# Kernel tuning notes

Hardware: AMD Instinct MI355X
Metric: run time of the kernel (lower is better)

## Reference

```python
import jax, jax.numpy as jnp
import numpy as np

DEPTH = 17                 # levels of the complete binary tree
N = 2**DEPTH - 1           # 131071 nodes, BFS order: children of n are 2n+1, 2n+2
IN_DIM = 128
HID = 128
OUT = 128


def setup_inputs() -> dict:
    key = jax.random.key(0)
    ks = jax.random.split(key, 20)

    def lin_w(k, o, i):
        s = 1.0 / np.sqrt(i)
        return jax.random.uniform(k, (o, i), minval=-s, maxval=s, dtype=jnp.float32)

    def lin_b(k, o, i):
        s = 1.0 / np.sqrt(i)
        return jax.random.uniform(k, (o,), minval=-s, maxval=s, dtype=jnp.float32)

    inp = {"x": jax.random.normal(ks[0], (N, IN_DIM), dtype=jnp.float32)}
    # complete binary tree, parent -> child edges (row0=src/parent, row1=dst/child)
    child = np.arange(1, N)
    parent = (child - 1) // 2
    inp["edge_index"] = jnp.asarray(np.stack([parent, child]), dtype=jnp.int32)
    names = [("Wi", "bWi", IN_DIM), ("Ui", "bUi", HID),
             ("Wf", "bWf", IN_DIM), ("Uf", "bUf", HID),
             ("Wo", "bWo", IN_DIM), ("Uo", "bUo", HID),
             ("Wu", "bWu", IN_DIM), ("Uu", "bUu", HID)]
    ki = 1
    for wname, bname, idim in names:
        inp[wname] = lin_w(ks[ki], HID, idim)
        inp[bname] = lin_b(ks[ki + 1], HID, idim)
        ki += 2
    inp["Wp"] = lin_w(ks[17], OUT, HID)
    inp["bWp"] = lin_b(ks[18], OUT, HID)
    return inp


def reference(x, edge_index, Wi, bWi, Ui, bUi, Wf, bWf, Uf, bUf,
              Wo, bWo, Uo, bUo, Wu, bWu, Uu, bUu, Wp, bWp):
    # edge_index encodes the complete binary tree in BFS order (children of n
    # are 2n+1 and 2n+2), so the recursion batches exactly by tree level.
    # Precompute input-side gate projections for ALL nodes in 4 GEMMs
    # (equivalent to calling W_*(x[node]) per node in the torch recursion).
    xi = x @ Wi.T + bWi            # (N, H)
    xf = x @ Wf.T + bWf
    xo = x @ Wo.T + bWo
    xu = x @ Wu.T + bWu

    h_next = None  # hidden states of the level below (children)
    c_next = None
    for d in range(DEPTH - 1, -1, -1):   # bottom-up over tree levels
        s = 2**d - 1                     # first node index of level d
        cnt = 2**d                       # nodes at level d
        li, lf, lo, lu = xi[s:s + cnt], xf[s:s + cnt], xo[s:s + cnt], xu[s:s + cnt]
        if h_next is None:               # leaves: no children, h_sum = 0
            i = jax.nn.sigmoid(li)
            o = jax.nn.sigmoid(lo)
            u = jnp.tanh(lu)
            c = i * u
        else:
            # children of node s+k are at positions 2(s+k)+1, 2(s+k)+2: contiguous
            ch_h = h_next.reshape(cnt, 2, HID)
            ch_c = c_next.reshape(cnt, 2, HID)
            h_sum = ch_h.sum(axis=1)     # child-sum
            i = jax.nn.sigmoid(li + h_sum @ Ui.T + bUi)
            o = jax.nn.sigmoid(lo + h_sum @ Uo.T + bUo)
            u = jnp.tanh(lu + h_sum @ Uu.T + bUu)
            # per-child forget gates: sigmoid(W_f x + U_f h_k)
            f = jax.nn.sigmoid(lf[:, None, :] + jnp.einsum('nkh,gh->nkg', ch_h, Uf) + bUf)
            c = i * u + (f * ch_c).sum(axis=1)
        h = o * jnp.tanh(c)
        h_next, c_next = h, c

    h_root = h_next[0]                   # root node index 0
    # dropout is identity in eval mode
    return h_root @ Wp.T + bWp           # (OUT,)
```

## Files before the change

### kernel.cpp

```cpp
#include <hip/hip_runtime.h>
#include <hip/hip_bf16.h>


#define DEPTH 17
#define NTREE ((1 << DEPTH) - 1)
#define DIM 128
#define XSTR 136
#define HSTR 136
#define CSTR 132

typedef __attribute__((ext_vector_type(8))) short short8;
typedef __attribute__((ext_vector_type(4))) float float4v;

__device__ __forceinline__ float sigm(float v) {
    return __fdividef(1.0f, 1.0f + __expf(-v));
}
__device__ __forceinline__ float ftanh(float v) {
    float e = __expf(2.0f * v);
    return 1.0f - __fdividef(2.0f, e + 1.0f);
}

__device__ __forceinline__ unsigned short f2bf(float f) {
    __bf16 h = (__bf16)f;
    unsigned short r;
    __builtin_memcpy(&r, &h, 2);
    return r;
}
__device__ __forceinline__ float bf2f(unsigned short s) {
    union { unsigned u; float f; } a; a.u = ((unsigned)s) << 16;
    return a.f;
}

struct WPtrs {
    const float* W[4];  const float* U[4];
    const float* bW[4]; const float* bU[4];
};

__global__ __launch_bounds__(256) void prep_kernel(WPtrs p, unsigned short* __restrict__ Bsw,
                                                   float* __restrict__ biasWU, float* __restrict__ biasL) {
    int idx = blockIdx.x * 256 + threadIdx.x;
    int j = idx & 7;
    int lane = (idx >> 3) & 63;
    int g = (idx >> 9) & 3;
    int ks = (idx >> 11) & 7;
    int w = idx >> 14;
    int L = lane & 15, q = lane >> 4;
    int c = w * 16 + L;
    int k = ks * 32 + q * 8 + j;
    float v = (k < 128) ? p.W[g][c * 128 + k] * (g == 3 ? 1.0f : 0.5f)
                        : p.U[g][c * 128 + (k - 128)];
    Bsw[idx] = f2bf(v);
    if (idx < 512) {
        int gg = idx >> 7, cc = idx & 127;
        biasWU[idx] = p.bW[gg][cc] + p.bU[gg][cc];
        biasL[idx]  = p.bW[gg][cc];
    }
}

__global__ __launch_bounds__(512, 2) void kd3_kernel(
    const float* __restrict__ x, const unsigned short* __restrict__ Bsw,
    const float* __restrict__ biasL, const float* __restrict__ biasWU,
    unsigned short* __restrict__ hbf, float* __restrict__ cbuf, int ntiles) {
    __shared__ __align__(16) unsigned short xs[2][56 * XSTR];
    __shared__ __align__(16) unsigned short h0[32 * XSTR];
    __shared__ __align__(16) unsigned short c0[32 * XSTR];
    __shared__ __align__(16) unsigned short h1[16 * XSTR];
    __shared__ __align__(16) unsigned short c1[16 * XSTR];
    __shared__ __align__(16) unsigned short hA2[8 * XSTR];
    __shared__ __align__(16) float cA2[8 * CSTR];

    const int tid = threadIdx.x;
    const int w = tid >> 6, lane = tid & 63, L = lane & 15, q = lane >> 4;
    const int ch = w * 16 + L;

    short8 b[32];
#pragma unroll
    for (int t = 0; t < 32; ++t)
        b[t] = *(const short8*)(Bsw + ((size_t)w << 14) + (t << 9) + lane * 8);

    float4 pfx[4];
    {
        const long tt = blockIdx.x;
#pragma unroll
        for (int k = 0; k < 4; ++k) {
            const int i = tid + 512 * k;
            if (i < 1792) {
                const int row = i >> 5, j = i & 31;
                const long node = (row < 32) ? (65535l + tt * 32 + row)
                                 : (row < 48) ? (32767l + tt * 16 + (row - 32))
                                              : (16383l + tt * 8 + (row - 48));
                pfx[k] = *(const float4*)(x + (size_t)node * DIM + j * 4);
            }
        }
    }

    for (int it = 0; it < ntiles; ++it) {
        const long tt = (long)it * gridDim.x + blockIdx.x;
        const int pc = it & 1;
        unsigned short* xsp = xs[pc];

#pragma unroll
        for (int k = 0; k < 4; ++k) {
            const int i = tid + 512 * k;
            if (i < 1792) {
                const int row = i >> 5, j = i & 31;
                ushort4 o;
                o.x = f2bf(pfx[k].x); o.y = f2bf(pfx[k].y);
                o.z = f2bf(pfx[k].z); o.w = f2bf(pfx[k].w);
                *(ushort4*)(xsp + row * XSTR + j * 4) = o;
            }
        }
        __syncthreads();

        if (it + 1 < ntiles) {
            const long tn = tt + gridDim.x;
#pragma unroll
            for (int k = 0; k < 4; ++k) {
                const int i = tid + 512 * k;
                if (i < 1792) {
                    const int row = i >> 5, j = i & 31;
                    const long node = (row < 32) ? (65535l + tn * 32 + row)
                                     : (row < 48) ? (32767l + tn * 16 + (row - 32))
                                                  : (16383l + tn * 8 + (row - 48));
                    pfx[k] = *(const float4*)(x + (size_t)node * DIM + j * 4);
                }
            }
        }

        if (it > 0) {
            const long pn2 = 16383l + (tt - gridDim.x) * 8;
            for (int i = tid; i < 8 * 16; i += 512) {
                const int row = i >> 4, g = i & 15;
                *(uint4*)(hbf + (size_t)(pn2 + row) * DIM + g * 8) = *(const uint4*)(hA2 + row * XSTR + g * 8);
            }
            for (int i = tid; i < 8 * 32; i += 512) {
                const int row = i >> 5, j = i & 31;
                *(float4*)(cbuf + (size_t)(pn2 + row) * DIM + j * 4) = *(const float4*)(cA2 + row * CSTR + j * 4);
            }
        }

        {
            float4v acc[2][3];
#pragma unroll
            for (int mm = 0; mm < 2; ++mm)
#pragma unroll
                for (int g = 0; g < 3; ++g) acc[mm][g] = (float4v){0.f, 0.f, 0.f, 0.f};
#pragma unroll
            for (int ks = 0; ks < 4; ++ks) {
                short8 a[2];
                a[0] = *(const short8*)(xsp + L * XSTR + ks * 32 + q * 8);
                a[1] = *(const short8*)(xsp + (16 + L) * XSTR + ks * 32 + q * 8);
#pragma unroll
                for (int g = 0; g < 3; ++g)
#pragma unroll
                    for (int mm = 0; mm < 2; ++mm)
                        acc[mm][g] = __builtin_amdgcn_mfma_f32_16x16x32_bf16(a[mm], b[ks * 4 + g], acc[mm][g], 0, 0, 0);
            }
#pragma unroll
            for (int mm = 0; mm < 2; ++mm)
#pragma unroll
                for (int r = 0; r < 4; ++r) {
                    const int nl = 16 * mm + q * 4 + r;
                    float iv = sigm(2.f * acc[mm][0][r] + biasL[ch]);
                    float ov = sigm(2.f * acc[mm][1][r] + biasL[128 + ch]);
                    float uv = ftanh(2.f * acc[mm][2][r] + biasL[256 + ch]);
                    float cv = iv * uv;
                    c0[nl * XSTR + ch] = f2bf(cv);
                    h0[nl * XSTR + ch] = f2bf(ov * ftanh(cv));
                }
        }
        __syncthreads();

        {
            float4v acc[2][4];
#pragma unroll
            for (int mm = 0; mm < 2; ++mm)
#pragma unroll
                for (int g = 0; g < 4; ++g) acc[mm][g] = (float4v){0.f, 0.f, 0.f, 0.f};
#pragma unroll
            for (int ks = 0; ks < 8; ++ks) {
                const int kk = ks * 32;
                short8 a[2];
#pragma unroll
                for (int mm = 0; mm < 2; ++mm) {
                    if (kk < 128)
                        a[mm] = *(const short8*)(xsp + (32 + 8 * mm + (L >> 1)) * XSTR + kk + q * 8);
                    else
                        a[mm] = *(const short8*)(h0 + (16 * mm + L) * XSTR + (kk - 128) + q * 8);
                }
#pragma unroll
                for (int g = 0; g < 4; ++g)
#pragma unroll
                    for (int mm = 0; mm < 2; ++mm)
                        acc[mm][g] = __builtin_amdgcn_mfma_f32_16x16x32_bf16(a[mm], b[ks * 4 + g], acc[mm][g], 0, 0, 0);
            }
#pragma unroll
            for (int mm = 0; mm < 2; ++mm)
#pragma unroll
                for (int e = 0; e < 2; ++e) {
                    const int nl = 8 * mm + 2 * q + e;
                    const int r0 = 2 * e, r1 = 2 * e + 1;
                    float iv = sigm(acc[mm][0][r0] + acc[mm][0][r1] + biasWU[ch]);
                    float ov = sigm(acc[mm][1][r0] + acc[mm][1][r1] + biasWU[128 + ch]);
                    float uv = ftanh(acc[mm][2][r0] + acc[mm][2][r1] + biasWU[256 + ch]);
                    float fl = sigm(acc[mm][3][r0] + biasWU[384 + ch]);
                    float fr = sigm(acc[mm][3][r1] + biasWU[384 + ch]);
                    float cl = bf2f(c0[(2 * nl) * XSTR + ch]);
                    float cr = bf2f(c0[(2 * nl + 1) * XSTR + ch]);
                    float cv = iv * uv + fl * cl + fr * cr;
                    c1[nl * XSTR + ch] = f2bf(cv);
                    h1[nl * XSTR + ch] = f2bf(ov * ftanh(cv));
                }
        }
        __syncthreads();

        {
            float4v acc[4];
#pragma unroll
            for (int g = 0; g < 4; ++g) acc[g] = (float4v){0.f, 0.f, 0.f, 0.f};
#pragma unroll
            for (int ks = 0; ks < 8; ++ks) {
                const int kk = ks * 32;
                short8 a;
                if (kk < 128)
                    a = *(const short8*)(xsp + (48 + (L >> 1)) * XSTR + kk + q * 8);
                else
                    a = *(const short8*)(h1 + L * XSTR + (kk - 128) + q * 8);
#pragma unroll
                for (int g = 0; g < 4; ++g)
                    acc[g] = __builtin_amdgcn_mfma_f32_16x16x32_bf16(a, b[ks * 4 + g], acc[g], 0, 0, 0);
            }
#pragma unroll
            for (int e = 0; e < 2; ++e) {
                const int nl = 2 * q + e;
                const int r0 = 2 * e, r1 = 2 * e + 1;
                float iv = sigm(acc[0][r0] + acc[0][r1] + biasWU[ch]);
                float ov = sigm(acc[1][r0] + acc[1][r1] + biasWU[128 + ch]);
                float uv = ftanh(acc[2][r0] + acc[2][r1] + biasWU[256 + ch]);
                float fl = sigm(acc[3][r0] + biasWU[384 + ch]);
                float fr = sigm(acc[3][r1] + biasWU[384 + ch]);
                float cl = bf2f(c1[(2 * nl) * XSTR + ch]);
                float cr = bf2f(c1[(2 * nl + 1) * XSTR + ch]);
                float cv = iv * uv + fl * cl + fr * cr;
                cA2[nl * CSTR + ch] = cv;
                hA2[nl * XSTR + ch] = f2bf(ov * ftanh(cv));
            }
        }
    }

    __syncthreads();
    {
        const long tl = (long)(ntiles - 1) * gridDim.x + blockIdx.x;
        const long n2 = 16383l + tl * 8;
        for (int i = tid; i < 8 * 16; i += 512) {
            const int row = i >> 4, g = i & 15;
            *(uint4*)(hbf + (size_t)(n2 + row) * DIM + g * 8) = *(const uint4*)(hA2 + row * XSTR + g * 8);
        }
        for (int i = tid; i < 8 * 32; i += 512) {
            const int row = i >> 5, j = i & 31;
            *(float4*)(cbuf + (size_t)(n2 + row) * DIM + j * 4) = *(const float4*)(cA2 + row * CSTR + j * 4);
        }
    }
}

template <bool LEAF0>
__global__ __launch_bounds__(512, 2) void kd2r_kernel(
    const float* __restrict__ x, const unsigned short* __restrict__ Bsw,
    const float* __restrict__ biasL, const float* __restrict__ biasWU,
    unsigned short* __restrict__ hbf, float* __restrict__ cbuf,
    int x0base, int x1base, int ntiles) {
    __shared__ __align__(16) unsigned short xs[2][48 * XSTR];
    __shared__ __align__(16) unsigned short hc[LEAF0 ? 16 : 64 * XSTR];
    __shared__ __align__(16) unsigned short h0[32 * XSTR];
    __shared__ __align__(16) unsigned short c0[32 * XSTR];
    __shared__ __align__(16) unsigned short hA1[16 * XSTR];
    __shared__ __align__(16) float cA1[16 * CSTR];

    const int tid = threadIdx.x;
    const int w = tid >> 6, lane = tid & 63, L = lane & 15, q = lane >> 4;
    const int ch = w * 16 + L;

    short8 b[32];
#pragma unroll
    for (int t = 0; t < 32; ++t)
        b[t] = *(const short8*)(Bsw + ((size_t)w << 14) + (t << 9) + lane * 8);

    float4 pfx[3];
    {
        const long tt = blockIdx.x;
        const long n0 = (long)x0base + tt * 32, n1 = (long)x1base + tt * 16;
#pragma unroll
        for (int k = 0; k < 3; ++k) {
            const int i = tid + 512 * k;
            const int row = i >> 5, j = i & 31;
            const long node = (row < 32) ? (n0 + row) : (n1 + (row - 32));
            pfx[k] = *(const float4*)(x + (size_t)node * DIM + j * 4);
        }
    }

    for (int it = 0; it < ntiles; ++it) {
        const long tt = (long)it * gridDim.x + blockIdx.x;
        const long n0 = (long)x0base + tt * 32;
        const long n1 = (long)x1base + tt * 16;
        const long cb = 2 * n0 + 1;
        const int pc = it & 1;
        unsigned short* xsp = xs[pc];

#pragma unroll
        for (int k = 0; k < 3; ++k) {
            const int i = tid + 512 * k;
            const int row = i >> 5, j = i & 31;
            ushort4 o;
            o.x = f2bf(pfx[k].x); o.y = f2bf(pfx[k].y);
            o.z = f2bf(pfx[k].z); o.w = f2bf(pfx[k].w);
            *(ushort4*)(xsp + row * XSTR + j * 4) = o;
        }
        if (!LEAF0) {
            for (int i = tid; i < 64 * 16; i += 512) {
                const int row = i >> 4, g = i & 15;
                *(uint4*)(hc + row * XSTR + g * 8) =
                    *(const uint4*)(hbf + (size_t)(cb + row) * DIM + g * 8);
            }
        }
        __syncthreads();

        if (it + 1 < ntiles) {
            const long tn = tt + gridDim.x;
            const long m0 = (long)x0base + tn * 32, m1 = (long)x1base + tn * 16;
#pragma unroll
            for (int k = 0; k < 3; ++k) {
                const int i = tid + 512 * k;
                const int row = i >> 5, j = i & 31;
                const long node = (row < 32) ? (m0 + row) : (m1 + (row - 32));
                pfx[k] = *(const float4*)(x + (size_t)node * DIM + j * 4);
            }
        }

        if (it > 0) {
            const long pn1 = n1 - (long)gridDim.x * 16;
            for (int i = tid; i < 16 * 16; i += 512) {
                const int row = i >> 4, g = i & 15;
                *(uint4*)(hbf + (size_t)(pn1 + row) * DIM + g * 8) = *(const uint4*)(hA1 + row * XSTR + g * 8);
            }
            for (int i = tid; i < 16 * 32; i += 512) {
                const int row = i >> 5, j = i & 31;
                *(float4*)(cbuf + (size_t)(pn1 + row) * DIM + j * 4) = *(const float4*)(cA1 + row * CSTR + j * 4);
            }
        }

        if (LEAF0) {
            float4v acc[2][3];
#pragma unroll
            for (int mm = 0; mm < 2; ++mm)
#pragma unroll
                for (int g = 0; g < 3; ++g) acc[mm][g] = (float4v){0.f, 0.f, 0.f, 0.f};
#pragma unroll
            for (int ks = 0; ks < 4; ++ks) {
                short8 a[2];
                a[0] = *(const short8*)(xsp + L * XSTR + ks * 32 + q * 8);
                a[1] = *(const short8*)(xsp + (16 + L) * XSTR + ks * 32 + q * 8);
#pragma unroll
                for (int g = 0; g < 3; ++g)
#pragma unroll
                    for (int mm = 0; mm < 2; ++mm)
                        acc[mm][g] = __builtin_amdgcn_mfma_f32_16x16x32_bf16(a[mm], b[ks * 4 + g], acc[mm][g], 0, 0, 0);
            }
#pragma unroll
            for (int mm = 0; mm < 2; ++mm)
#pragma unroll
                for (int r = 0; r < 4; ++r) {
                    const int nl = 16 * mm + q * 4 + r;
                    float iv = sigm(2.f * acc[mm][0][r] + biasL[ch]);
                    float ov = sigm(2.f * acc[mm][1][r] + biasL[128 + ch]);
                    float uv = ftanh(2.f * acc[mm][2][r] + biasL[256 + ch]);
                    float cv = iv * uv;
                    c0[nl * XSTR + ch] = f2bf(cv);
                    h0[nl * XSTR + ch] = f2bf(ov * ftanh(cv));
                }
        } else {
            for (int mc = 0; mc < 4; mc += 2) {
                float4v acc[2][4];
#pragma unroll
                for (int mm = 0; mm < 2; ++mm)
#pragma unroll
                    for (int g = 0; g < 4; ++g) acc[mm][g] = (float4v){0.f, 0.f, 0.f, 0.f};
#pragma unroll
                for (int ks = 0; ks < 8; ++ks) {
                    const int kk = ks * 32;
                    short8 a[2];
#pragma unroll
                    for (int mm = 0; mm < 2; ++mm) {
                        if (kk < 128)
                            a[mm] = *(const short8*)(xsp + (8 * (mc + mm) + (L >> 1)) * XSTR + kk + q * 8);
                        else
                            a[mm] = *(const short8*)(hc + (16 * (mc + mm) + L) * XSTR + (kk - 128) + q * 8);
                    }
#pragma unroll
                    for (int g = 0; g < 4; ++g)
#pragma unroll
                        for (int mm = 0; mm < 2; ++mm)
                            acc[mm][g] = __builtin_amdgcn_mfma_f32_16x16x32_bf16(a[mm], b[ks * 4 + g], acc[mm][g], 0, 0, 0);
                }
#pragma unroll
                for (int mm = 0; mm < 2; ++mm)
#pragma unroll
                    for (int e = 0; e < 2; ++e) {
                        const int nl = 8 * (mc + mm) + 2 * q + e;
                        const int r0 = 2 * e, r1 = 2 * e + 1;
                        float iv = sigm(acc[mm][0][r0] + acc[mm][0][r1] + biasWU[ch]);
                        float ov = sigm(acc[mm][1][r0] + acc[mm][1][r1] + biasWU[128 + ch]);
                        float uv = ftanh(acc[mm][2][r0] + acc[mm][2][r1] + biasWU[256 + ch]);
                        float fl = sigm(acc[mm][3][r0] + biasWU[384 + ch]);
                        float fr = sigm(acc[mm][3][r1] + biasWU[384 + ch]);
                        float cl = cbuf[(size_t)(cb + 2 * nl) * DIM + ch];
                        float cr = cbuf[(size_t)(cb + 2 * nl + 1) * DIM + ch];
                        float cv = iv * uv + fl * cl + fr * cr;
                        c0[nl * XSTR + ch] = f2bf(cv);
                        h0[nl * XSTR + ch] = f2bf(ov * ftanh(cv));
                    }
            }
        }
        __syncthreads();

        {
            float4v acc[2][4];
#pragma unroll
            for (int mm = 0; mm < 2; ++mm)
#pragma unroll
                for (int g = 0; g < 4; ++g) acc[mm][g] = (float4v){0.f, 0.f, 0.f, 0.f};
#pragma unroll
            for (int ks = 0; ks < 8; ++ks) {
                const int kk = ks * 32;
                short8 a[2];
#pragma unroll
                for (int mm = 0; mm < 2; ++mm) {
                    if (kk < 128)
                        a[mm] = *(const short8*)(xsp + (32 + 8 * mm + (L >> 1)) * XSTR + kk + q * 8);
                    else
                        a[mm] = *(const short8*)(h0 + (16 * mm + L) * XSTR + (kk - 128) + q * 8);
                }
#pragma unroll
                for (int g = 0; g < 4; ++g)
#pragma unroll
                    for (int mm = 0; mm < 2; ++mm)
                        acc[mm][g] = __builtin_amdgcn_mfma_f32_16x16x32_bf16(a[mm], b[ks * 4 + g], acc[mm][g], 0, 0, 0);
            }
#pragma unroll
            for (int mm = 0; mm < 2; ++mm)
#pragma unroll
                for (int e = 0; e < 2; ++e) {
                    const int nl = 8 * mm + 2 * q + e;
                    const int r0 = 2 * e, r1 = 2 * e + 1;
                    float iv = sigm(acc[mm][0][r0] + acc[mm][0][r1] + biasWU[ch]);
                    float ov = sigm(acc[mm][1][r0] + acc[mm][1][r1] + biasWU[128 + ch]);
                    float uv = ftanh(acc[mm][2][r0] + acc[mm][2][r1] + biasWU[256 + ch]);
                    float fl = sigm(acc[mm][3][r0] + biasWU[384 + ch]);
                    float fr = sigm(acc[mm][3][r1] + biasWU[384 + ch]);
                    float cl = bf2f(c0[(2 * nl) * XSTR + ch]);
                    float cr = bf2f(c0[(2 * nl + 1) * XSTR + ch]);
                    float cv = iv * uv + fl * cl + fr * cr;
                    cA1[nl * CSTR + ch] = cv;
                    hA1[nl * XSTR + ch] = f2bf(ov * ftanh(cv));
                }
        }
    }

    __syncthreads();
    {
        const long tl = (long)(ntiles - 1) * gridDim.x + blockIdx.x;
        const long n1 = (long)x1base + tl * 16;
        for (int i = tid; i < 16 * 16; i += 512) {
            const int row = i >> 4, g = i & 15;
            *(uint4*)(hbf + (size_t)(n1 + row) * DIM + g * 8) = *(const uint4*)(hA1 + row * XSTR + g * 8);
        }
        for (int i = tid; i < 16 * 32; i += 512) {
            const int row = i >> 5, j = i & 31;
            *(float4*)(cbuf + (size_t)(n1 + row) * DIM + j * 4) = *(const float4*)(cA1 + row * CSTR + j * 4);
        }
    }
}

template <bool GCH>
__device__ __forceinline__ void internal_level(
    const unsigned short* xc,
    const unsigned short* hin_l, const float* cin_l,
    const unsigned short* __restrict__ hin_g, const float* __restrict__ cin_g, long cb,
    unsigned short* ho, int ho_str, float* co, int co_str, int cnt,
    const short8 (&b)[32], const float* __restrict__ biasWU,
    int L, int q, int ch) {
    const int rows = 2 * cnt;
    const int mt = (rows + 15) >> 4;
    for (int mc = 0; mc < mt; mc += 2) {
        const int mm_n = (mt - mc >= 2) ? 2 : 1;
        float4v acc[2][4];
#pragma unroll
        for (int mm = 0; mm < 2; ++mm)
#pragma unroll
            for (int g = 0; g < 4; ++g) acc[mm][g] = (float4v){0.f, 0.f, 0.f, 0.f};
#pragma unroll
        for (int ks = 0; ks < 8; ++ks) {
            const int kk = ks * 32;
            short8 a[2];
#pragma unroll
            for (int mm = 0; mm < 2; ++mm) {
                if (mm < mm_n) {
                    if (kk < 128) {
                        int xr = 8 * (mc + mm) + (L >> 1);
                        if (xr >= cnt) xr = 0;
                        a[mm] = *(const short8*)(xc + xr * XSTR + kk + q * 8);
                    } else if (!GCH) {
                        a[mm] = *(const short8*)(hin_l + (16 * (mc + mm) + L) * HSTR + (kk - 128) + q * 8);
                    } else {
                        a[mm] = *(const short8*)(hin_g + (size_t)(cb + 16 * (mc + mm) + L) * DIM + (kk - 128) + q * 8);
                    }
                }
            }
#pragma unroll
            for (int g = 0; g < 4; ++g)
#pragma unroll
                for (int mm = 0; mm < 2; ++mm)
                    if (mm < mm_n)
                        acc[mm][g] = __builtin_amdgcn_mfma_f32_16x16x32_bf16(a[mm], b[ks * 4 + g], acc[mm][g], 0, 0, 0);
        }
#pragma unroll
        for (int mm = 0; mm < 2; ++mm)
#pragma unroll
            for (int e = 0; e < 2; ++e) {
                if (mm < mm_n) {
                    const int nl = 8 * (mc + mm) + 2 * q + e;
                    if (nl < cnt) {
                        const int r0 = 2 * e, r1 = 2 * e + 1;
                        float iv = sigm(acc[mm][0][r0] + acc[mm][0][r1] + biasWU[ch]);
                        float ov = sigm(acc[mm][1][r0] + acc[mm][1][r1] + biasWU[128 + ch]);
                        float uv = ftanh(acc[mm][2][r0] + acc[mm][2][r1] + biasWU[256 + ch]);
                        float fl = sigm(acc[mm][3][r0] + biasWU[384 + ch]);
                        float fr = sigm(acc[mm][3][r1] + biasWU[384 + ch]);
                        float cl, cr;
                        if (!GCH) {
                            cl = cin_l[(2 * nl) * CSTR + ch];
                            cr = cin_l[(2 * nl + 1) * CSTR + ch];
                        } else {
                            cl = cin_g[(size_t)(cb + 2 * nl) * DIM + ch];
                            cr = cin_g[(size_t)(cb + 2 * nl + 1) * DIM + ch];
                        }
                        float cv = iv * uv + fl * cl + fr * cr;
                        co[nl * co_str + ch] = cv;
                        ho[nl * ho_str + ch] = f2bf(ov * ftanh(cv));
                    }
                }
            }
    }
}

template <int C, int NL, bool PROJ>
__global__ __launch_bounds__(512, 2) void k23_kernel(
    const float* __restrict__ x, const unsigned short* __restrict__ Bsw,
    const float* __restrict__ biasWU, unsigned short* __restrict__ hbf,
    float* __restrict__ cbuf, int d0,
    const float* __restrict__ Wp, const float* __restrict__ bWp,
    float* __restrict__ out) {
    constexpr int TOTX = 2 * C - (C >> (NL - 1));
    constexpr int AR = (C < 16) ? 16 : C;
    __shared__ __align__(16) unsigned short xs[TOTX * XSTR];
    __shared__ __align__(16) unsigned short hA[AR * HSTR];
    __shared__ __align__(16) unsigned short hB[16 * HSTR];
    __shared__ __align__(16) float cA[AR * CSTR];
    __shared__ __align__(16) float cB[16 * CSTR];
    __shared__ float red[4][128];

    const int tid = threadIdx.x;
    const int w = tid >> 6, lane = tid & 63, L = lane & 15, q = lane >> 4;
    const int ch = w * 16 + L;

    short8 b[32];
#pragma unroll
    for (int t = 0; t < 32; ++t)
        b[t] = *(const short8*)(Bsw + ((size_t)w << 14) + (t << 9) + lane * 8);

    {
        int xoff = 0;
#pragma unroll
        for (int l = 0; l < NL; ++l) {
            const int rows = C >> l;
            const long base = ((1 << (d0 - l)) - 1) + (long)blockIdx.x * rows;
            for (int i = tid; i < rows * 32; i += 512) {
                const int row = i >> 5, j = i & 31;
                float4 v = *(const float4*)(x + (size_t)(base + row) * DIM + j * 4);
                ushort4 o;
                o.x = f2bf(v.x); o.y = f2bf(v.y); o.z = f2bf(v.z); o.w = f2bf(v.w);
                *(ushort4*)(xs + (xoff + row) * XSTR + j * 4) = o;
            }
            xoff += rows;
        }
    }
    __syncthreads();

    const long cb = ((1 << (d0 + 1)) - 1) + (long)blockIdx.x * (2 * C);
    internal_level<true>(xs, nullptr, nullptr, hbf, cbuf, cb,
                         hA, HSTR, cA, CSTR, C, b, biasWU, L, q, ch);
    __syncthreads();

    const unsigned short* hin = hA;
    const float* cin = cA;
    int xoff = C;
#pragma unroll
    for (int l = 1; l < NL; ++l) {
        const int cnt = C >> l;
        if (!PROJ && l == NL - 1) {
            const long ob = ((1 << (d0 - (NL - 1))) - 1) + (long)blockIdx.x;
            internal_level<false>(xs + xoff * XSTR, hin, cin, nullptr, nullptr, 0,
                                  hbf + (size_t)ob * DIM, DIM,
                                  cbuf + (size_t)ob * DIM, DIM, cnt, b, biasWU, L, q, ch);
        } else {
            unsigned short* ho = (l & 1) ? hB : hA;
            float* co = (l & 1) ? cB : cA;
            internal_level<false>(xs + xoff * XSTR, hin, cin, nullptr, nullptr, 0,
                                  ho, HSTR, co, CSTR, cnt, b, biasWU, L, q, ch);
            __syncthreads();
            hin = ho; cin = co;
        }
        xoff += cnt;
    }

    if (PROJ) {
        const int o = tid & 127, sg = tid >> 7;
        float pacc = 0.f;
#pragma unroll
        for (int jj = 0; jj < 8; ++jj) {
            const int k = sg * 32 + jj * 4;
            float4 wv = *(const float4*)(Wp + o * DIM + k);
            pacc += bf2f(hin[k]) * wv.x + bf2f(hin[k + 1]) * wv.y +
                    bf2f(hin[k + 2]) * wv.z + bf2f(hin[k + 3]) * wv.w;
        }
        red[sg][o] = pacc;
        __syncthreads();
        if (tid < 128) out[tid] = bWp[tid] + red[0][tid] + red[1][tid] + red[2][tid] + red[3][tid];
    }
}

extern "C" void kernel_launch(void* const* d_in, const int* in_sizes, int n_in,
                              void* d_out, int out_size, void* d_ws, size_t ws_size,
                              hipStream_t stream) {
    const float* x   = (const float*)d_in[0];
    const float* Wi  = (const float*)d_in[2];  const float* bWi = (const float*)d_in[3];
    const float* Ui  = (const float*)d_in[4];  const float* bUi = (const float*)d_in[5];
    const float* Wf  = (const float*)d_in[6];  const float* bWf = (const float*)d_in[7];
    const float* Uf  = (const float*)d_in[8];  const float* bUf = (const float*)d_in[9];
    const float* Wo  = (const float*)d_in[10]; const float* bWo = (const float*)d_in[11];
    const float* Uo  = (const float*)d_in[12]; const float* bUo = (const float*)d_in[13];
    const float* Wu  = (const float*)d_in[14]; const float* bWu = (const float*)d_in[15];
    const float* Uu  = (const float*)d_in[16]; const float* bUu = (const float*)d_in[17];
    const float* Wp  = (const float*)d_in[18]; const float* bWp = (const float*)d_in[19];

    unsigned short* Bsw = (unsigned short*)d_ws;
    float* biasWU = (float*)(Bsw + 131072);
    float* biasL  = biasWU + 512;
    float* cbuf   = biasL + 512;
    unsigned short* hbf = (unsigned short*)(cbuf + (size_t)65536 * DIM);

    WPtrs p;
    p.W[0] = Wi; p.W[1] = Wo; p.W[2] = Wu; p.W[3] = Wf;
    p.U[0] = Ui; p.U[1] = Uo; p.U[2] = Uu; p.U[3] = Uf;
    p.bW[0] = bWi; p.bW[1] = bWo; p.bW[2] = bWu; p.bW[3] = bWf;
    p.bU[0] = bUi; p.bU[1] = bUo; p.bU[2] = bUu; p.bU[3] = bUf;

    prep_kernel<<<512, 256, 0, stream>>>(p, Bsw, biasWU, biasL);

    kd3_kernel<<<256, 512, 0, stream>>>(x, Bsw, biasL, biasWU, hbf, cbuf, 8);
    kd2r_kernel<false><<<256, 512, 0, stream>>>(x, Bsw, biasL, biasWU, hbf, cbuf,
                                                (1 << 13) - 1, (1 << 12) - 1, 1);
    kd2r_kernel<false><<<64, 512, 0, stream>>>(x, Bsw, biasL, biasWU, hbf, cbuf,
                                               (1 << 11) - 1, (1 << 10) - 1, 1);
    k23_kernel<16, 5, false><<<32, 512, 0, stream>>>(x, Bsw, biasWU, hbf, cbuf, 9,
                                                     nullptr, nullptr, nullptr);
    k23_kernel<16, 5, true><<<1, 512, 0, stream>>>(x, Bsw, biasWU, hbf, cbuf, 4,
                                                   Wp, bWp, (float*)d_out);
}
```

Baseline: 244.8 us.

## Precompute W·x for upper levels in a separate GEMM kernel, drop prep kernel

Removes the weight-prep kernel: each kernel now packs W/U rows to bf16 in registers directly from fp32 inputs. A new wx_kernel computes the input-side gate projections for the upper 16K nodes up front, so the upper-level kernels multiply only by U over K=128 instead of K=256. The launch sequence is also regrouped from five tree kernels into four larger ones (32x6 level blocks). This shortens the serial chain of small upper-level kernels. In exchange it adds an fp32 wx buffer written to and read back from global memory, and redundant weight packing in every block.

```diff
diff --git a/kernel.cpp b/kernel.cpp
--- a/kernel.cpp
+++ b/kernel.cpp
@@ -2,8 +2,6 @@
 #include <hip/hip_bf16.h>
 
 
-#define DEPTH 17
-#define NTREE ((1 << DEPTH) - 1)
 #define DIM 128
 #define XSTR 136
 #define HSTR 136
@@ -19,7 +17,6 @@
     float e = __expf(2.0f * v);
     return 1.0f - __fdividef(2.0f, e + 1.0f);
 }
-
 __device__ __forceinline__ unsigned short f2bf(float f) {
     __bf16 h = (__bf16)f;
     unsigned short r;
@@ -36,30 +33,71 @@
     const float* bW[4]; const float* bU[4];
 };
 
-__global__ __launch_bounds__(256) void prep_kernel(WPtrs p, unsigned short* __restrict__ Bsw,
-                                                   float* __restrict__ biasWU, float* __restrict__ biasL) {
-    int idx = blockIdx.x * 256 + threadIdx.x;
-    int j = idx & 7;
-    int lane = (idx >> 3) & 63;
-    int g = (idx >> 9) & 3;
-    int ks = (idx >> 11) & 7;
-    int w = idx >> 14;
-    int L = lane & 15, q = lane >> 4;
-    int c = w * 16 + L;
-    int k = ks * 32 + q * 8 + j;
-    float v = (k < 128) ? p.W[g][c * 128 + k] * (g == 3 ? 1.0f : 0.5f)
-                        : p.U[g][c * 128 + (k - 128)];
-    Bsw[idx] = f2bf(v);
-    if (idx < 512) {
-        int gg = idx >> 7, cc = idx & 127;
-        biasWU[idx] = p.bW[gg][cc] + p.bU[gg][cc];
-        biasL[idx]  = p.bW[gg][cc];
-    }
-}
-
-__global__ __launch_bounds__(512, 2) void kd3_kernel(
-    const float* __restrict__ x, const unsigned short* __restrict__ Bsw,
-    const float* __restrict__ biasL, const float* __restrict__ biasWU,
+__device__ __forceinline__ short8 packrow(const float* __restrict__ src, float s) {
+    float4 v0 = *(const float4*)src, v1 = *(const float4*)(src + 4);
+    short8 r;
+    r[0] = (short)f2bf(v0.x * s); r[1] = (short)f2bf(v0.y * s);
+    r[2] = (short)f2bf(v0.z * s); r[3] = (short)f2bf(v0.w * s);
+    r[4] = (short)f2bf(v1.x * s); r[5] = (short)f2bf(v1.y * s);
+    r[6] = (short)f2bf(v1.z * s); r[7] = (short)f2bf(v1.w * s);
+    return r;
+}
+
+__global__ __launch_bounds__(512) void wx_kernel(const float* __restrict__ x, WPtrs p,
+                                                 float* __restrict__ wx) {
+    __shared__ __align__(16) unsigned short xsw[32 * XSTR];
+    const int tid = threadIdx.x;
+    const int w = tid >> 6, lane = tid & 63, L = lane & 15, q = lane >> 4;
+    const int ch = w * 16 + L;
+
+    short8 bw[16];
+#pragma unroll
+    for (int ks = 0; ks < 4; ++ks)
+#pragma unroll
+        for (int g = 0; g < 4; ++g)
+            bw[ks * 4 + g] = packrow(p.W[g] + ch * 128 + ks * 32 + q * 8, 1.0f);
+    float bW0 = p.bW[0][ch], bW1 = p.bW[1][ch], bW2 = p.bW[2][ch], bW3 = p.bW[3][ch];
+
+    const long nb = (long)blockIdx.x * 32;
+    for (int i = tid; i < 32 * 32; i += 512) {
+        const int row = i >> 5, j = i & 31;
+        float4 v = *(const float4*)(x + (size_t)(nb + row) * DIM + j * 4);
+        ushort4 o;
+        o.x = f2bf(v.x); o.y = f2bf(v.y); o.z = f2bf(v.z); o.w = f2bf(v.w);
+        *(ushort4*)(xsw + row * XSTR + j * 4) = o;
+    }
+    __syncthreads();
+
+    float4v acc[2][4];
+#pragma unroll
+    for (int mm = 0; mm < 2; ++mm)
+#pragma unroll
+        for (int g = 0; g < 4; ++g) acc[mm][g] = (float4v){0.f, 0.f, 0.f, 0.f};
+#pragma unroll
+    for (int ks = 0; ks < 4; ++ks) {
+        short8 a0 = *(const short8*)(xsw + L * XSTR + ks * 32 + q * 8);
+        short8 a1 = *(const short8*)(xsw + (16 + L) * XSTR + ks * 32 + q * 8);
+#pragma unroll
+        for (int g = 0; g < 4; ++g) {
+            acc[0][g] = __builtin_amdgcn_mfma_f32_16x16x32_bf16(a0, bw[ks * 4 + g], acc[0][g], 0, 0, 0);
+            acc[1][g] = __builtin_amdgcn_mfma_f32_16x16x32_bf16(a1, bw[ks * 4 + g], acc[1][g], 0, 0, 0);
+        }
+    }
+#pragma unroll
+    for (int mm = 0; mm < 2; ++mm)
+#pragma unroll
+        for (int r = 0; r < 4; ++r) {
+            const long node = nb + 16 * mm + q * 4 + r;
+            float* o = wx + node * 512 + ch;
+            o[0]   = acc[mm][0][r] + bW0;
+            o[128] = acc[mm][1][r] + bW1;
+            o[256] = acc[mm][2][r] + bW2;
+            o[384] = acc[mm][3][r] + bW3;
+        }
+}
+
+__global__ __launch_bounds__(512, 2) void kd3f_kernel(
+    const float* __restrict__ x, WPtrs p,
     unsigned short* __restrict__ hbf, float* __restrict__ cbuf, int ntiles) {
     __shared__ __align__(16) unsigned short xs[2][56 * XSTR];
     __shared__ __align__(16) unsigned short h0[32 * XSTR];
@@ -75,8 +113,15 @@
 
     short8 b[32];
 #pragma unroll
-    for (int t = 0; t < 32; ++t)
-        b[t] = *(const short8*)(Bsw + ((size_t)w << 14) + (t << 9) + lane * 8);
+    for (int ks = 0; ks < 8; ++ks)
+#pragma unroll
+        for (int g = 0; g < 4; ++g)
+            b[ks * 4 + g] = (ks < 4)
+                ? packrow(p.W[g] + ch * 128 + ks * 32 + q * 8, (g == 3) ? 1.0f : 0.5f)
+                : packrow(p.U[g] + ch * 128 + (ks - 4) * 32 + q * 8, 1.0f);
+    const float bLi = p.bW[0][ch], bLo = p.bW[1][ch], bLu = p.bW[2][ch];
+    const float bWUi = bLi + p.bU[0][ch], bWUo = bLo + p.bU[1][ch];
+    const float bWUu = bLu + p.bU[2][ch], bWUf = p.bW[3][ch] + p.bU[3][ch];
 
     float4 pfx[4];
     {
@@ -161,9 +206,9 @@
 #pragma unroll
                 for (int r = 0; r < 4; ++r) {
                     const int nl = 16 * mm + q * 4 + r;
-                    float iv = sigm(2.f * acc[mm][0][r] + biasL[ch]);
-                    float ov = sigm(2.f * acc[mm][1][r] + biasL[128 + ch]);
-                    float uv = ftanh(2.f * acc[mm][2][r] + biasL[256 + ch]);
+                    float iv = sigm(2.f * acc[mm][0][r] + bLi);
+                    float ov = sigm(2.f * acc[mm][1][r] + bLo);
+                    float uv = ftanh(2.f * acc[mm][2][r] + bLu);
                     float cv = iv * uv;
                     c0[nl * XSTR + ch] = f2bf(cv);
                     h0[nl * XSTR + ch] = f2bf(ov * ftanh(cv));
@@ -200,11 +245,11 @@
                 for (int e = 0; e < 2; ++e) {
                     const int nl = 8 * mm + 2 * q + e;
                     const int r0 = 2 * e, r1 = 2 * e + 1;
-                    float iv = sigm(acc[mm][0][r0] + acc[mm][0][r1] + biasWU[ch]);
-                    float ov = sigm(acc[mm][1][r0] + acc[mm][1][r1] + biasWU[128 + ch]);
-                    float uv = ftanh(acc[mm][2][r0] + acc[mm][2][r1] + biasWU[256 + ch]);
-                    float fl = sigm(acc[mm][3][r0] + biasWU[384 + ch]);
-                    float fr = sigm(acc[mm][3][r1] + biasWU[384 + ch]);
+                    float iv = sigm(acc[mm][0][r0] + acc[mm][0][r1] + bWUi);
+                    float ov = sigm(acc[mm][1][r0] + acc[mm][1][r1] + bWUo);
+                    float uv = ftanh(acc[mm][2][r0] + acc[mm][2][r1] + bWUu);
+                    float fl = sigm(acc[mm][3][r0] + bWUf);
+                    float fr = sigm(acc[mm][3][r1] + bWUf);
                     float cl = bf2f(c0[(2 * nl) * XSTR + ch]);
                     float cr = bf2f(c0[(2 * nl + 1) * XSTR + ch]);
                     float cv = iv * uv + fl * cl + fr * cr;
@@ -234,11 +279,11 @@
             for (int e = 0; e < 2; ++e) {
                 const int nl = 2 * q + e;
                 const int r0 = 2 * e, r1 = 2 * e + 1;
-                float iv = sigm(acc[0][r0] + acc[0][r1] + biasWU[ch]);
-                float ov = sigm(acc[1][r0] + acc[1][r1] + biasWU[128 + ch]);
-                float uv = ftanh(acc[2][r0] + acc[2][r1] + biasWU[256 + ch]);
-                float fl = sigm(acc[3][r0] + biasWU[384 + ch]);
-                float fr = sigm(acc[3][r1] + biasWU[384 + ch]);
+                float iv = sigm(acc[0][r0] + acc[0][r1] + bWUi);
+                float ov = sigm(acc[1][r0] + acc[1][r1] + bWUo);
+                float uv = ftanh(acc[2][r0] + acc[2][r1] + bWUu);
+                float fl = sigm(acc[3][r0] + bWUf);
+                float fr = sigm(acc[3][r1] + bWUf);
                 float cl = bf2f(c1[(2 * nl) * XSTR + ch]);
                 float cr = bf2f(c1[(2 * nl + 1) * XSTR + ch]);
                 float cv = iv * uv + fl * cl + fr * cr;
@@ -263,14 +308,10 @@
     }
 }
 
-template <bool LEAF0>
-__global__ __launch_bounds__(512, 2) void kd2r_kernel(
-    const float* __restrict__ x, const unsigned short* __restrict__ Bsw,
-    const float* __restrict__ biasL, const float* __restrict__ biasWU,
-    unsigned short* __restrict__ hbf, float* __restrict__ cbuf,
-    int x0base, int x1base, int ntiles) {
-    __shared__ __align__(16) unsigned short xs[2][48 * XSTR];
-    __shared__ __align__(16) unsigned short hc[LEAF0 ? 16 : 64 * XSTR];
+__global__ __launch_bounds__(512, 2) void kd2u_kernel(
+    WPtrs p, const float* __restrict__ wx,
+    unsigned short* __restrict__ hbf, float* __restrict__ cbuf) {
+    __shared__ __align__(16) unsigned short hc[64 * XSTR];
     __shared__ __align__(16) unsigned short h0[32 * XSTR];
     __shared__ __align__(16) unsigned short c0[32 * XSTR];
     __shared__ __align__(16) unsigned short hA1[16 * XSTR];
@@ -280,213 +321,120 @@
     const int w = tid >> 6, lane = tid & 63, L = lane & 15, q = lane >> 4;
     const int ch = w * 16 + L;
 
-    short8 b[32];
-#pragma unroll
-    for (int t = 0; t < 32; ++t)
-        b[t] = *(const short8*)(Bsw + ((size_t)w << 14) + (t << 9) + lane * 8);
-
-    float4 pfx[3];
+    short8 b[16];
+#pragma unroll
+    for (int ks = 0; ks < 4; ++ks)
+#pragma unroll
+        for (int g = 0; g < 4; ++g)
+            b[ks * 4 + g] = packrow(p.U[g] + ch * 128 + ks * 32 + q * 8, 1.0f);
+    const float bUi = p.bU[0][ch], bUo = p.bU[1][ch], bUu = p.bU[2][ch], bUf = p.bU[3][ch];
+
+    const long tt = blockIdx.x;
+    const long n0 = 8191l + tt * 32;
+    const long n1 = 4095l + tt * 16;
+    const long cb = 2 * n0 + 1;
+
+    for (int i = tid; i < 64 * 16; i += 512) {
+        const int row = i >> 4, g = i & 15;
+        *(uint4*)(hc + row * XSTR + g * 8) = *(const uint4*)(hbf + (size_t)(cb + row) * DIM + g * 8);
+    }
+    __syncthreads();
+
+    for (int mc = 0; mc < 4; mc += 2) {
+        float4v acc[2][4];
+#pragma unroll
+        for (int mm = 0; mm < 2; ++mm)
+#pragma unroll
+            for (int g = 0; g < 4; ++g) acc[mm][g] = (float4v){0.f, 0.f, 0.f, 0.f};
+#pragma unroll
+        for (int ks = 0; ks < 4; ++ks) {
+            short8 a[2];
+#pragma unroll
+            for (int mm = 0; mm < 2; ++mm)
+                a[mm] = *(const short8*)(hc + (16 * (mc + mm) + L) * XSTR + ks * 32 + q * 8);
+#pragma unroll
+            for (int g = 0; g < 4; ++g)
+#pragma unroll
+                for (int mm = 0; mm < 2; ++mm)
+                    acc[mm][g] = __builtin_amdgcn_mfma_f32_16x16x32_bf16(a[mm], b[ks * 4 + g], acc[mm][g], 0, 0, 0);
+        }
+#pragma unroll
+        for (int mm = 0; mm < 2; ++mm)
+#pragma unroll
+            for (int e = 0; e < 2; ++e) {
+                const int nl = 8 * (mc + mm) + 2 * q + e;
+                const int r0 = 2 * e, r1 = 2 * e + 1;
+                const float* wp = wx + (n0 + nl) * 512 + ch;
+                float iv = sigm(acc[mm][0][r0] + acc[mm][0][r1] + wp[0] + bUi);
+                float ov = sigm(acc[mm][1][r0] + acc[mm][1][r1] + wp[128] + bUo);
+                float uv = ftanh(acc[mm][2][r0] + acc[mm][2][r1] + wp[256] + bUu);
+                float fl = sigm(acc[mm][3][r0] + wp[384] + bUf);
+                float fr = sigm(acc[mm][3][r1] + wp[384] + bUf);
+                float cl = cbuf[(size_t)(cb + 2 * nl) * DIM + ch];
+                float cr = cbuf[(size_t)(cb + 2 * nl + 1) * DIM + ch];
+                float cv = iv * uv + fl * cl + fr * cr;
+                c0[nl * XSTR + ch] = f2bf(cv);
+                h0[nl * XSTR + ch] = f2bf(ov * ftanh(cv));
+            }
+    }
+    __syncthreads();
+
     {
-        const long tt = blockIdx.x;
-        const long n0 = (long)x0base + tt * 32, n1 = (long)x1base + tt * 16;
-#pragma unroll
-        for (int k = 0; k < 3; ++k) {
-            const int i = tid + 512 * k;
-            const int row = i >> 5, j = i & 31;
-            const long node = (row < 32) ? (n0 + row) : (n1 + (row - 32));
-            pfx[k] = *(const float4*)(x + (size_t)node * DIM + j * 4);
-        }
-    }
-
-    for (int it = 0; it < ntiles; ++it) {
-        const long tt = (long)it * gridDim.x + blockIdx.x;
-        const long n0 = (long)x0base + tt * 32;
-        const long n1 = (long)x1base + tt * 16;
-        const long cb = 2 * n0 + 1;
-        const int pc = it & 1;
-        unsigned short* xsp = xs[pc];
-
-#pragma unroll
-        for (int k = 0; k < 3; ++k) {
-            const int i = tid + 512 * k;
-            const int row = i >> 5, j = i & 31;
-            ushort4 o;
-            o.x = f2bf(pfx[k].x); o.y = f2bf(pfx[k].y);
-            o.z = f2bf(pfx[k].z); o.w = f2bf(pfx[k].w);
-            *(ushort4*)(xsp + row * XSTR + j * 4) = o;
-        }
-        if (!LEAF0) {
-            for (int i = tid; i < 64 * 16; i += 512) {
-                const int row = i >> 4, g = i & 15;
-                *(uint4*)(hc + row * XSTR + g * 8) =
-                    *(const uint4*)(hbf + (size_t)(cb + row) * DIM + g * 8);
-            }
-        }
-        __syncthreads();
-
-        if (it + 1 < ntiles) {
-            const long tn = tt + gridDim.x;
-            const long m0 = (long)x0base + tn * 32, m1 = (long)x1base + tn * 16;
-#pragma unroll
-            for (int k = 0; k < 3; ++k) {
-                const int i = tid + 512 * k;
-                const int row = i >> 5, j = i & 31;
-                const long node = (row < 32) ? (m0 + row) : (m1 + (row - 32));
-                pfx[k] = *(const float4*)(x + (size_t)node * DIM + j * 4);
-            }
-        }
-
-        if (it > 0) {
-            const long pn1 = n1 - (long)gridDim.x * 16;
-            for (int i = tid; i < 16 * 16; i += 512) {
-                const int row = i >> 4, g = i & 15;
-                *(uint4*)(hbf + (size_t)(pn1 + row) * DIM + g * 8) = *(const uint4*)(hA1 + row * XSTR + g * 8);
-            }
-            for (int i = tid; i < 16 * 32; i += 512) {
-                const int row = i >> 5, j = i & 31;
-                *(float4*)(cbuf + (size_t)(pn1 + row) * DIM + j * 4) = *(const float4*)(cA1 + row * CSTR + j * 4);
-            }
-        }
-
-        if (LEAF0) {
-            float4v acc[2][3];
+        float4v acc[2][4];
+#pragma unroll
+        for (int mm = 0; mm < 2; ++mm)
+#pragma unroll
+            for (int g = 0; g < 4; ++g) acc[mm][g] = (float4v){0.f, 0.f, 0.f, 0.f};
+#pragma unroll
+        for (int ks = 0; ks < 4; ++ks) {
+            short8 a[2];
 #pragma unroll
             for (int mm = 0; mm < 2; ++mm)
-#pragma unroll
-                for (int g = 0; g < 3; ++g) acc[mm][g] = (float4v){0.f, 0.f, 0.f, 0.f};
-#pragma unroll
-            for (int ks = 0; ks < 4; ++ks) {
-                short8 a[2];
-                a[0] = *(const short8*)(xsp + L * XSTR + ks * 32 + q * 8);
-                a[1] = *(const short8*)(xsp + (16 + L) * XSTR + ks * 32 + q * 8);
-#pragma unroll
-                for (int g = 0; g < 3; ++g)
-#pragma unroll
-                    for (int mm = 0; mm < 2; ++mm)
-                        acc[mm][g] = __builtin_amdgcn_mfma_f32_16x16x32_bf16(a[mm], b[ks * 4 + g], acc[mm][g], 0, 0, 0);
-            }
-#pragma unroll
-            for (int mm = 0; mm < 2; ++mm)
-#pragma unroll
-                for (int r = 0; r < 4; ++r) {
-                    const int nl = 16 * mm + q * 4 + r;
-                    float iv = sigm(2.f * acc[mm][0][r] + biasL[ch]);
-                    float ov = sigm(2.f * acc[mm][1][r] + biasL[128 + ch]);
-                    float uv = ftanh(2.f * acc[mm][2][r] + biasL[256 + ch]);
-                    float cv = iv * uv;
-                    c0[nl * XSTR + ch] = f2bf(cv);
-                    h0[nl * XSTR + ch] = f2bf(ov * ftanh(cv));
-                }
-        } else {
-            for (int mc = 0; mc < 4; mc += 2) {
-                float4v acc[2][4];
+                a[mm] = *(const short8*)(h0 + (16 * mm + L) * XSTR + ks * 32 + q * 8);
+#pragma unroll
+            for (int g = 0; g < 4; ++g)
 #pragma unroll
                 for (int mm = 0; mm < 2; ++mm)
-#pragma unroll
-                    for (int g = 0; g < 4; ++g) acc[mm][g] = (float4v){0.f, 0.f, 0.f, 0.f};
-#pragma unroll
-                for (int ks = 0; ks < 8; ++ks) {
-                    const int kk = ks * 32;
-                    short8 a[2];
-#pragma unroll
-                    for (int mm = 0; mm < 2; ++mm) {
-                        if (kk < 128)
-                            a[mm] = *(const short8*)(xsp + (8 * (mc + mm) + (L >> 1)) * XSTR + kk + q * 8);
-                        else
-                            a[mm] = *(const short8*)(hc + (16 * (mc + mm) + L) * XSTR + (kk - 128) + q * 8);
-                    }
-#pragma unroll
-                    for (int g = 0; g < 4; ++g)
-#pragma unroll
-                        for (int mm = 0; mm < 2; ++mm)
-                            acc[mm][g] = __builtin_amdgcn_mfma_f32_16x16x32_bf16(a[mm], b[ks * 4 + g], acc[mm][g], 0, 0, 0);
-                }
-#pragma unroll
-                for (int mm = 0; mm < 2; ++mm)
-#pragma unroll
-                    for (int e = 0; e < 2; ++e) {
-                        const int nl = 8 * (mc + mm) + 2 * q + e;
-                        const int r0 = 2 * e, r1 = 2 * e + 1;
-                        float iv = sigm(acc[mm][0][r0] + acc[mm][0][r1] + biasWU[ch]);
-                        float ov = sigm(acc[mm][1][r0] + acc[mm][1][r1] + biasWU[128 + ch]);
-                        float uv = ftanh(acc[mm][2][r0] + acc[mm][2][r1] + biasWU[256 + ch]);
-                        float fl = sigm(acc[mm][3][r0] + biasWU[384 + ch]);
-                        float fr = sigm(acc[mm][3][r1] + biasWU[384 + ch]);
-                        float cl = cbuf[(size_t)(cb + 2 * nl) * DIM + ch];
-                        float cr = cbuf[(size_t)(cb + 2 * nl + 1) * DIM + ch];
-                        float cv = iv * uv + fl * cl + fr * cr;
-                        c0[nl * XSTR + ch] = f2bf(cv);
-                        h0[nl * XSTR + ch] = f2bf(ov * ftanh(cv));
-                    }
-            }
-        }
-        __syncthreads();
-
-        {
-            float4v acc[2][4];
-#pragma unroll
-            for (int mm = 0; mm < 2; ++mm)
-#pragma unroll
-                for (int g = 0; g < 4; ++g) acc[mm][g] = (float4v){0.f, 0.f, 0.f, 0.f};
-#pragma unroll
-            for (int ks = 0; ks < 8; ++ks) {
-                const int kk = ks * 32;
-                short8 a[2];
-#pragma unroll
-                for (int mm = 0; mm < 2; ++mm) {
-                    if (kk < 128)
-                        a[mm] = *(const short8*)(xsp + (32 + 8 * mm + (L >> 1)) * XSTR + kk + q * 8);
-                    else
-                        a[mm] = *(const short8*)(h0 + (16 * mm + L) * XSTR + (kk - 128) + q * 8);
-                }
-#pragma unroll
-                for (int g = 0; g < 4; ++g)
-#pragma unroll
-                    for (int mm = 0; mm < 2; ++mm)
-                        acc[mm][g] = __builtin_amdgcn_mfma_f32_16x16x32_bf16(a[mm], b[ks * 4 + g], acc[mm][g], 0, 0, 0);
-            }
-#pragma unroll
-            for (int mm = 0; mm < 2; ++mm)
-#pragma unroll
-                for (int e = 0; e < 2; ++e) {
-                    const int nl = 8 * mm + 2 * q + e;
-                    const int r0 = 2 * e, r1 = 2 * e + 1;
-                    float iv = sigm(acc[mm][0][r0] + acc[mm][0][r1] + biasWU[ch]);
-                    float ov = sigm(acc[mm][1][r0] + acc[mm][1][r1] + biasWU[128 + ch]);
-                    float uv = ftanh(acc[mm][2][r0] + acc[mm][2][r1] + biasWU[256 + ch]);
-                    float fl = sigm(acc[mm][3][r0] + biasWU[384 + ch]);
-                    float fr = sigm(acc[mm][3][r1] + biasWU[384 + ch]);
-                    float cl = bf2f(c0[(2 * nl) * XSTR + ch]);
-                    float cr = bf2f(c0[(2 * nl + 1) * XSTR + ch]);
-                    float cv = iv * uv + fl * cl + fr * cr;
-                    cA1[nl * CSTR + ch] = cv;
-                    hA1[nl * XSTR + ch] = f2bf(ov * ftanh(cv));
-                }
-        }
-    }
-
+                    acc[mm][g] = __builtin_amdgcn_mfma_f32_16x16x32_bf16(a[mm], b[ks * 4 + g], acc[mm][g], 0, 0, 0);
+        }
+#pragma unroll
+        for (int mm = 0; mm < 2; ++mm)
+#pragma unroll
+            for (int e = 0; e < 2; ++e) {
+                const int nl = 8 * mm + 2 * q + e;
+                const int r0 = 2 * e, r1 = 2 * e + 1;
+                const float* wp = wx + (n1 + nl) * 512 + ch;
+                float iv = sigm(acc[mm][0][r0] + acc[mm][0][r1] + wp[0] + bUi);
+                float ov = sigm(acc[mm][1][r0] + acc[mm][1][r1] + wp[128] + bUo);
+                float uv = ftanh(acc[mm][2][r0] + acc[mm][2][r1] + wp[256] + bUu);
+                float fl = sigm(acc[mm][3][r0] + wp[384] + bUf);
+                float fr = sigm(acc[mm][3][r1] + wp[384] + bUf);
+                float cl = bf2f(c0[(2 * nl) * XSTR + ch]);
+                float cr = bf2f(c0[(2 * nl + 1) * XSTR + ch]);
+                float cv = iv * uv + fl * cl + fr * cr;
+                cA1[nl * CSTR + ch] = cv;
+                hA1[nl * XSTR + ch] = f2bf(ov * ftanh(cv));
+            }
+    }
     __syncthreads();
-    {
-        const long tl = (long)(ntiles - 1) * gridDim.x + blockIdx.x;
-        const long n1 = (long)x1base + tl * 16;
-        for (int i = tid; i < 16 * 16; i += 512) {
-            const int row = i >> 4, g = i & 15;
-            *(uint4*)(hbf + (size_t)(n1 + row) * DIM + g * 8) = *(const uint4*)(hA1 + row * XSTR + g * 8);
-        }
-        for (int i = tid; i < 16 * 32; i += 512) {
-            const int row = i >> 5, j = i & 31;
-            *(float4*)(cbuf + (size_t)(n1 + row) * DIM + j * 4) = *(const float4*)(cA1 + row * CSTR + j * 4);
-        }
+
+    for (int i = tid; i < 16 * 16; i += 512) {
+        const int row = i >> 4, g = i & 15;
+        *(uint4*)(hbf + (size_t)(n1 + row) * DIM + g * 8) = *(const uint4*)(hA1 + row * XSTR + g * 8);
+    }
+    for (int i = tid; i < 16 * 32; i += 512) {
+        const int row = i >> 5, j = i & 31;
+        *(float4*)(cbuf + (size_t)(n1 + row) * DIM + j * 4) = *(const float4*)(cA1 + row * CSTR + j * 4);
     }
 }
 
 template <bool GCH>
-__device__ __forceinline__ void internal_level(
-    const unsigned short* xc,
+__device__ __forceinline__ void internal_level_u(
     const unsigned short* hin_l, const float* cin_l,
     const unsigned short* __restrict__ hin_g, const float* __restrict__ cin_g, long cb,
+    const float* __restrict__ wx, long nbase,
     unsigned short* ho, int ho_str, float* co, int co_str, int cnt,
-    const short8 (&b)[32], const float* __restrict__ biasWU,
+    const short8 (&b)[16], float bUi, float bUo, float bUu, float bUf,
     int L, int q, int ch) {
     const int rows = 2 * cnt;
     const int mt = (rows + 15) >> 4;
@@ -498,21 +446,15 @@
 #pragma unroll
             for (int g = 0; g < 4; ++g) acc[mm][g] = (float4v){0.f, 0.f, 0.f, 0.f};
 #pragma unroll
-        for (int ks = 0; ks < 8; ++ks) {
-            const int kk = ks * 32;
+        for (int ks = 0; ks < 4; ++ks) {
             short8 a[2];
 #pragma unroll
             for (int mm = 0; mm < 2; ++mm) {
                 if (mm < mm_n) {
-                    if (kk < 128) {
-                        int xr = 8 * (mc + mm) + (L >> 1);
-                        if (xr >= cnt) xr = 0;
-                        a[mm] = *(const short8*)(xc + xr * XSTR + kk + q * 8);
-                    } else if (!GCH) {
-                        a[mm] = *(const short8*)(hin_l + (16 * (mc + mm) + L) * HSTR + (kk - 128) + q * 8);
-                    } else {
-                        a[mm] = *(const short8*)(hin_g + (size_t)(cb + 16 * (mc + mm) + L) * DIM + (kk - 128) + q * 8);
-                    }
+                    if (!GCH)
+                        a[mm] = *(const short8*)(hin_l + (16 * (mc + mm) + L) * HSTR + ks * 32 + q * 8);
+                    else
+                        a[mm] = *(const short8*)(hin_g + (size_t)(cb + 16 * (mc + mm) + L) * DIM + ks * 32 + q * 8);
                 }
             }
 #pragma unroll
@@ -530,11 +472,12 @@
                     const int nl = 8 * (mc + mm) + 2 * q + e;
                     if (nl < cnt) {
                         const int r0 = 2 * e, r1 = 2 * e + 1;
-                        float iv = sigm(acc[mm][0][r0] + acc[mm][0][r1] + biasWU[ch]);
-                        float ov = sigm(acc[mm][1][r0] + acc[mm][1][r1] + biasWU[128 + ch]);
-                        float uv = ftanh(acc[mm][2][r0] + acc[mm][2][r1] + biasWU[256 + ch]);
-                        float fl = sigm(acc[mm][3][r0] + biasWU[384 + ch]);
-                        float fr = sigm(acc[mm][3][r1] + biasWU[384 + ch]);
+                        const float* wp = wx + (nbase + nl) * 512 + ch;
+                        float iv = sigm(acc[mm][0][r0] + acc[mm][0][r1] + wp[0] + bUi);
+                        float ov = sigm(acc[mm][1][r0] + acc[mm][1][r1] + wp[128] + bUo);
+                        float uv = ftanh(acc[mm][2][r0] + acc[mm][2][r1] + wp[256] + bUu);
+                        float fl = sigm(acc[mm][3][r0] + wp[384] + bUf);
+                        float fr = sigm(acc[mm][3][r1] + wp[384] + bUf);
                         float cl, cr;
                         if (!GCH) {
                             cl = cin_l[(2 * nl) * CSTR + ch];
@@ -553,73 +496,57 @@
 }
 
 template <int C, int NL, bool PROJ>
-__global__ __launch_bounds__(512, 2) void k23_kernel(
-    const float* __restrict__ x, const unsigned short* __restrict__ Bsw,
-    const float* __restrict__ biasWU, unsigned short* __restrict__ hbf,
-    float* __restrict__ cbuf, int d0,
+__global__ __launch_bounds__(512, 2) void k23u_kernel(
+    WPtrs p, const float* __restrict__ wx,
+    unsigned short* __restrict__ hbf, float* __restrict__ cbuf, int d0,
     const float* __restrict__ Wp, const float* __restrict__ bWp,
     float* __restrict__ out) {
-    constexpr int TOTX = 2 * C - (C >> (NL - 1));
     constexpr int AR = (C < 16) ? 16 : C;
-    __shared__ __align__(16) unsigned short xs[TOTX * XSTR];
     __shared__ __align__(16) unsigned short hA[AR * HSTR];
-    __shared__ __align__(16) unsigned short hB[16 * HSTR];
+    __shared__ __align__(16) unsigned short hB[((C / 2) < 16 ? 16 : (C / 2)) * HSTR];
     __shared__ __align__(16) float cA[AR * CSTR];
-    __shared__ __align__(16) float cB[16 * CSTR];
+    __shared__ __align__(16) float cB[((C / 2) < 16 ? 16 : (C / 2)) * CSTR];
     __shared__ float red[4][128];
 
     const int tid = threadIdx.x;
     const int w = tid >> 6, lane = tid & 63, L = lane & 15, q = lane >> 4;
     const int ch = w * 16 + L;
 
-    short8 b[32];
-#pragma unroll
-    for (int t = 0; t < 32; ++t)
-        b[t] = *(const short8*)(Bsw + ((size_t)w << 14) + (t << 9) + lane * 8);
-
-    {
-        int xoff = 0;
-#pragma unroll
-        for (int l = 0; l < NL; ++l) {
-            const int rows = C >> l;
-            const long base = ((1 << (d0 - l)) - 1) + (long)blockIdx.x * rows;
-            for (int i = tid; i < rows * 32; i += 512) {
-                const int row = i >> 5, j = i & 31;
-                float4 v = *(const float4*)(x + (size_t)(base + row) * DIM + j * 4);
-                ushort4 o;
-                o.x = f2bf(v.x); o.y = f2bf(v.y); o.z = f2bf(v.z); o.w = f2bf(v.w);
-                *(ushort4*)(xs + (xoff + row) * XSTR + j * 4) = o;
-            }
-            xoff += rows;
-        }
-    }
-    __syncthreads();
-
-    const long cb = ((1 << (d0 + 1)) - 1) + (long)blockIdx.x * (2 * C);
-    internal_level<true>(xs, nullptr, nullptr, hbf, cbuf, cb,
-                         hA, HSTR, cA, CSTR, C, b, biasWU, L, q, ch);
+    short8 b[16];
+#pragma unroll
+    for (int ks = 0; ks < 4; ++ks)
+#pragma unroll
+        for (int g = 0; g < 4; ++g)
+            b[ks * 4 + g] = packrow(p.U[g] + ch * 128 + ks * 32 + q * 8, 1.0f);
+    const float bUi = p.bU[0][ch], bUo = p.bU[1][ch], bUu = p.bU[2][ch], bUf = p.bU[3][ch];
+
+    const int bx = blockIdx.x;
+    const long cb = ((1l << (d0 + 1)) - 1) + (long)bx * (2 * C);
+    const long nb0 = ((1l << d0) - 1) + (long)bx * C;
+    internal_level_u<true>(nullptr, nullptr, hbf, cbuf, cb, wx, nb0,
+                           hA, HSTR, cA, CSTR, C, b, bUi, bUo, bUu, bUf, L, q, ch);
     __syncthreads();
 
     const unsigned short* hin = hA;
     const float* cin = cA;
-    int xoff = C;
 #pragma unroll
     for (int l = 1; l < NL; ++l) {
         const int cnt = C >> l;
+        const long nb = ((1l << (d0 - l)) - 1) + (long)bx * cnt;
         if (!PROJ && l == NL - 1) {
-            const long ob = ((1 << (d0 - (NL - 1))) - 1) + (long)blockIdx.x;
-            internal_level<false>(xs + xoff * XSTR, hin, cin, nullptr, nullptr, 0,
-                                  hbf + (size_t)ob * DIM, DIM,
-                                  cbuf + (size_t)ob * DIM, DIM, cnt, b, biasWU, L, q, ch);
+            internal_level_u<false>(hin, cin, nullptr, nullptr, 0, wx, nb,
+                                    hbf + (size_t)nb * DIM, DIM,
+                                    cbuf + (size_t)nb * DIM, DIM, cnt,
+                                    b, bUi, bUo, bUu, bUf, L, q, ch);
         } else {
             unsigned short* ho = (l & 1) ? hB : hA;
             float* co = (l & 1) ? cB : cA;
-            internal_level<false>(xs + xoff * XSTR, hin, cin, nullptr, nullptr, 0,
-                                  ho, HSTR, co, CSTR, cnt, b, biasWU, L, q, ch);
+            internal_level_u<false>(hin, cin, nullptr, nullptr, 0, wx, nb,
+                                    ho, HSTR, co, CSTR, cnt,
+                                    b, bUi, bUo, bUu, bUf, L, q, ch);
             __syncthreads();
             hin = ho; cin = co;
         }
-        xoff += cnt;
     }
 
     if (PROJ) {
@@ -652,11 +579,9 @@
     const float* Uu  = (const float*)d_in[16]; const float* bUu = (const float*)d_in[17];
     const float* Wp  = (const float*)d_in[18]; const float* bWp = (const float*)d_in[19];
 
-    unsigned short* Bsw = (unsigned short*)d_ws;
-    float* biasWU = (float*)(Bsw + 131072);
-    float* biasL  = biasWU + 512;
-    float* cbuf   = biasL + 512;
-    unsigned short* hbf = (unsigned short*)(cbuf + (size_t)65536 * DIM);
+    float* cbuf = (float*)d_ws;
+    unsigned short* hbf = (unsigned short*)(cbuf + (size_t)32768 * DIM);
+    float* wx = (float*)(hbf + (size_t)32768 * DIM);
 
     WPtrs p;
     p.W[0] = Wi; p.W[1] = Wo; p.W[2] = Wu; p.W[3] = Wf;
@@ -664,15 +589,11 @@
     p.bW[0] = bWi; p.bW[1] = bWo; p.bW[2] = bWu; p.bW[3] = bWf;
     p.bU[0] = bUi; p.bU[1] = bUo; p.bU[2] = bUu; p.bU[3] = bUf;
 
-    prep_kernel<<<512, 256, 0, stream>>>(p, Bsw, biasWU, biasL);
-
-    kd3_kernel<<<256, 512, 0, stream>>>(x, Bsw, biasL, biasWU, hbf, cbuf, 8);
-    kd2r_kernel<false><<<256, 512, 0, stream>>>(x, Bsw, biasL, biasWU, hbf, cbuf,
-                                                (1 << 13) - 1, (1 << 12) - 1, 1);
-    kd2r_kernel<false><<<64, 512, 0, stream>>>(x, Bsw, biasL, biasWU, hbf, cbuf,
-                                               (1 << 11) - 1, (1 << 10) - 1, 1);
-    k23_kernel<16, 5, false><<<32, 512, 0, stream>>>(x, Bsw, biasWU, hbf, cbuf, 9,
-                                                     nullptr, nullptr, nullptr);
-    k23_kernel<16, 5, true><<<1, 512, 0, stream>>>(x, Bsw, biasWU, hbf, cbuf, 4,
-                                                   Wp, bWp, (float*)d_out);
-}
+    wx_kernel<<<512, 512, 0, stream>>>(x, p, wx);
+    kd3f_kernel<<<256, 512, 0, stream>>>(x, p, hbf, cbuf, 8);
+    kd2u_kernel<<<256, 512, 0, stream>>>(p, wx, hbf, cbuf);
+    k23u_kernel<32, 6, false><<<64, 512, 0, stream>>>(p, wx, hbf, cbuf, 11,
+                                                      nullptr, nullptr, nullptr);
+    k23u_kernel<32, 6, true><<<1, 512, 0, stream>>>(p, wx, hbf, cbuf, 5,
+                                                    Wp, bWp, (float*)d_out);
+}
```

Measured after the change: 321.3 us. 31.3% more time.
